# Kernel optimization log

Measured on AMD Instinct MI355X. Metric: run time of the kernel, lower is better.

Reference implementation:

```python
import jax, jax.numpy as jnp
import numpy as np

N_NODES = 50000
N_EDGES = 400000
IN_DIM = 512
OUT_DIM = 512


def setup_inputs() -> dict:
    key = jax.random.key(0)
    k1, k2, k3, k4 = jax.random.split(key, 4)
    x = jax.random.normal(k1, (N_NODES, IN_DIM), dtype=jnp.float32)
    edge_index = jax.random.randint(k2, (2, N_EDGES), 0, N_NODES, dtype=jnp.int64)
    # nn.Linear(in_dim, out_dim): weight [out, in], bias [out]
    W = jax.random.normal(k3, (OUT_DIM, IN_DIM), dtype=jnp.float32) / np.sqrt(IN_DIM)
    b = jax.random.normal(k4, (OUT_DIM,), dtype=jnp.float32) * 0.01
    return {"x": x, "edge_index": edge_index, "W": W, "b": b}


def reference(x, edge_index, W, b):
    n = x.shape[0]
    loops = jnp.arange(n, dtype=edge_index.dtype)
    row = jnp.concatenate([edge_index[0], loops])  # src
    col = jnp.concatenate([edge_index[1], loops])  # dst
    # degree from row counts (matches torch.bincount(row)); self-loops ensure deg >= 1
    deg = jax.ops.segment_sum(jnp.ones(row.shape[0], dtype=x.dtype), row, num_segments=n)
    dis = jax.lax.rsqrt(deg)  # deg^-0.5
    norm = dis[row] * dis[col]  # [E+N]
    h = x @ W.T + b  # [N, out_dim]
    # out[dst] += norm * h[src], fused gather-scale-scatter
    out = jax.ops.segment_sum(norm[:, None] * h[row], col, num_segments=n)
    return jax.nn.relu(out)
```

## Files before the change

kernel.cpp:

```cpp
#include <hip/hip_runtime.h>
#include <hip/hip_bf16.h>

#define K_DIM 512
#define N_DIM 512

typedef __attribute__((ext_vector_type(8))) short s8v;
typedef __attribute__((ext_vector_type(4))) short s4v;
typedef __attribute__((ext_vector_type(4))) float f4v;

__device__ __forceinline__ short f2bf(float f) {
  union { float f; unsigned u; } v; v.f = f;
  unsigned r = (v.u + 0x7FFFu + ((v.u >> 16) & 1u)) >> 16;
  return (short)r;
}
__device__ __forceinline__ float bflo(unsigned u) {
  union { unsigned u; float f; } v; v.u = u << 16; return v.f;
}
__device__ __forceinline__ float bfhi(unsigned u) {
  union { unsigned u; float f; } v; v.u = u & 0xffff0000u; return v.f;
}

__device__ __forceinline__ void gload16(const void* g, void* l) {
  __builtin_amdgcn_global_load_lds(
      (const __attribute__((address_space(1))) void*)g,
      (__attribute__((address_space(3))) void*)l, 16, 0, 0);
}

__global__ void k_flag(const int* __restrict__ e32, int* __restrict__ flag) {
  int t = threadIdx.x;
  int v = e32[2 * t + 1];
  unsigned long long m = __ballot(v == 0);
  if (t == 0) flag[0] = (m == ~0ULL) ? 1 : 0;
}

__global__ void k_convW(const float* __restrict__ W, short* __restrict__ Wb) {
  int i = (blockIdx.x * blockDim.x + threadIdx.x) * 4;
  float4 f = *(const float4*)(W + i);
  s4v s; s[0] = f2bf(f.x); s[1] = f2bf(f.y); s[2] = f2bf(f.z); s[3] = f2bf(f.w);
  *(s4v*)(Wb + i) = s;
}

__global__ void k_hist(const int* __restrict__ e32, const int* __restrict__ flag,
                       int* __restrict__ outdeg, int* __restrict__ indeg, int E) {
  int i = blockIdx.x * blockDim.x + threadIdx.x;
  if (i >= E) return;
  int st = flag[0] ? 2 : 1;
  int r = e32[(size_t)i * st];
  int c = e32[(size_t)(E + i) * st];
  atomicAdd(&outdeg[r], 1);
  atomicAdd(&indeg[c], 1);
}

__global__ void k_dis(const int* __restrict__ outdeg, float* __restrict__ dis, int n) {
  int i = blockIdx.x * blockDim.x + threadIdx.x;
  if (i < n) dis[i] = rsqrtf((float)(outdeg[i] + 1));
}

__global__ void k_scan_a(const int* __restrict__ in, int* __restrict__ part, int n) {
  __shared__ int sm[256];
  int i = blockIdx.x * 256 + threadIdx.x;
  sm[threadIdx.x] = (i < n) ? in[i] : 0;
  __syncthreads();
  for (int off = 128; off > 0; off >>= 1) {
    if (threadIdx.x < off) sm[threadIdx.x] += sm[threadIdx.x + off];
    __syncthreads();
  }
  if (threadIdx.x == 0) part[blockIdx.x] = sm[0];
}

__global__ void k_scan_b(int* __restrict__ part, int nb, int* __restrict__ row_start, int n) {
  __shared__ int sm[256];
  int t = threadIdx.x;
  int v = (t < nb) ? part[t] : 0;
  sm[t] = v; __syncthreads();
  for (int off = 1; off < 256; off <<= 1) {
    int a = (t >= off) ? sm[t - off] : 0;
    __syncthreads();
    sm[t] += a;
    __syncthreads();
  }
  part[t] = sm[t] - v;
  if (t == 255) row_start[n] = sm[255];
}

__global__ void k_scan_c(const int* __restrict__ in, const int* __restrict__ part,
                         int* __restrict__ row_start, int* __restrict__ cursor, int n) {
  __shared__ int sm[256];
  int i = blockIdx.x * 256 + threadIdx.x;
  int v = (i < n) ? in[i] : 0;
  sm[threadIdx.x] = v; __syncthreads();
  for (int off = 1; off < 256; off <<= 1) {
    int a = (threadIdx.x >= off) ? sm[threadIdx.x - off] : 0;
    __syncthreads();
    sm[threadIdx.x] += a;
    __syncthreads();
  }
  if (i < n) {
    int excl = part[blockIdx.x] + sm[threadIdx.x] - v;
    row_start[i] = excl;
    cursor[i] = excl;
  }
}

__global__ void k_fill(const int* __restrict__ e32, const int* __restrict__ flag,
                       int* __restrict__ cursor, int* __restrict__ csr, int E) {
  int i = blockIdx.x * blockDim.x + threadIdx.x;
  if (i >= E) return;
  int st = flag[0] ? 2 : 1;
  int r = e32[(size_t)i * st];
  int c = e32[(size_t)(E + i) * st];
  int p = atomicAdd(&cursor[c], 1);
  csr[p] = r;
}

__global__ __launch_bounds__(256) void k_gemm(const float* __restrict__ x,
    const short* __restrict__ Wb, const float* __restrict__ bias,
    short* __restrict__ h, int M) {
  __shared__ __align__(16) short As[2][128][40];
  __shared__ __align__(16) short Bs[2][128][32];
  const int n0 = blockIdx.x * 128;
  const int m0 = blockIdx.y * 128;
  const int tid = threadIdx.x;
  const int lane = tid & 63;
  const int wv = tid >> 6, wr = wv >> 1, wc = wv & 1;
  const int la = lane & 15, lg = lane >> 4;
  const int sr = tid >> 1, sc = (tid & 1) * 16;
  const float* xrow = x + (size_t)(m0 + sr) * K_DIM + sc;
  const bool aok = (m0 + sr) < M;
  const short* bsrc = Wb + (size_t)(n0 + (tid >> 2)) * K_DIM + (tid & 3) * 8;
  char* bdst0 = (char*)&Bs[0][0][0] + wv * 1024;
  char* bdst1 = (char*)&Bs[1][0][0] + wv * 1024;

  f4v acc[4][4] = {};

  gload16(bsrc, bdst0);
  gload16(bsrc + (size_t)64 * K_DIM, bdst0 + 4096);
  {
    float4 f0{}, f1{}, f2{}, f3{};
    if (aok) {
      f0 = *(const float4*)(xrow);
      f1 = *(const float4*)(xrow + 4);
      f2 = *(const float4*)(xrow + 8);
      f3 = *(const float4*)(xrow + 12);
    }
    s8v v0, v1;
    v0[0] = f2bf(f0.x); v0[1] = f2bf(f0.y); v0[2] = f2bf(f0.z); v0[3] = f2bf(f0.w);
    v0[4] = f2bf(f1.x); v0[5] = f2bf(f1.y); v0[6] = f2bf(f1.z); v0[7] = f2bf(f1.w);
    v1[0] = f2bf(f2.x); v1[1] = f2bf(f2.y); v1[2] = f2bf(f2.z); v1[3] = f2bf(f2.w);
    v1[4] = f2bf(f3.x); v1[5] = f2bf(f3.y); v1[6] = f2bf(f3.z); v1[7] = f2bf(f3.w);
    *(s8v*)&As[0][sr][sc] = v0;
    *(s8v*)&As[0][sr][sc + 8] = v1;
  }
  __syncthreads();

  for (int kt = 0; kt < 16; ++kt) {
    const int cur = kt & 1;
    const int nxt = cur ^ 1;
    float4 f0{}, f1{}, f2{}, f3{};
    if (kt < 15) {
      const int kk = (kt + 1) * 32;
      char* bd = cur ? bdst0 : bdst1;
      gload16(bsrc + kk, bd);
      gload16(bsrc + kk + (size_t)64 * K_DIM, bd + 4096);
      if (aok) {
        f0 = *(const float4*)(xrow + kk);
        f1 = *(const float4*)(xrow + kk + 4);
        f2 = *(const float4*)(xrow + kk + 8);
        f3 = *(const float4*)(xrow + kk + 12);
      }
    }
    s8v a0 = *(const s8v*)&As[cur][64 * wr + la][8 * lg];
    s8v a1 = *(const s8v*)&As[cur][64 * wr + 16 + la][8 * lg];
    s8v a2 = *(const s8v*)&As[cur][64 * wr + 32 + la][8 * lg];
    s8v a3 = *(const s8v*)&As[cur][64 * wr + 48 + la][8 * lg];
    s8v b0 = *(const s8v*)&Bs[cur][64 * wc + la][8 * lg];
    s8v b1 = *(const s8v*)&Bs[cur][64 * wc + 16 + la][8 * lg];
    s8v b2 = *(const s8v*)&Bs[cur][64 * wc + 32 + la][8 * lg];
    s8v b3 = *(const s8v*)&Bs[cur][64 * wc + 48 + la][8 * lg];
    acc[0][0] = __builtin_amdgcn_mfma_f32_16x16x32_bf16(a0, b0, acc[0][0], 0, 0, 0);
    acc[0][1] = __builtin_amdgcn_mfma_f32_16x16x32_bf16(a0, b1, acc[0][1], 0, 0, 0);
    acc[0][2] = __builtin_amdgcn_mfma_f32_16x16x32_bf16(a0, b2, acc[0][2], 0, 0, 0);
    acc[0][3] = __builtin_amdgcn_mfma_f32_16x16x32_bf16(a0, b3, acc[0][3], 0, 0, 0);
    acc[1][0] = __builtin_amdgcn_mfma_f32_16x16x32_bf16(a1, b0, acc[1][0], 0, 0, 0);
    acc[1][1] = __builtin_amdgcn_mfma_f32_16x16x32_bf16(a1, b1, acc[1][1], 0, 0, 0);
    acc[1][2] = __builtin_amdgcn_mfma_f32_16x16x32_bf16(a1, b2, acc[1][2], 0, 0, 0);
    acc[1][3] = __builtin_amdgcn_mfma_f32_16x16x32_bf16(a1, b3, acc[1][3], 0, 0, 0);
    acc[2][0] = __builtin_amdgcn_mfma_f32_16x16x32_bf16(a2, b0, acc[2][0], 0, 0, 0);
    acc[2][1] = __builtin_amdgcn_mfma_f32_16x16x32_bf16(a2, b1, acc[2][1], 0, 0, 0);
    acc[2][2] = __builtin_amdgcn_mfma_f32_16x16x32_bf16(a2, b2, acc[2][2], 0, 0, 0);
    acc[2][3] = __builtin_amdgcn_mfma_f32_16x16x32_bf16(a2, b3, acc[2][3], 0, 0, 0);
    acc[3][0] = __builtin_amdgcn_mfma_f32_16x16x32_bf16(a3, b0, acc[3][0], 0, 0, 0);
    acc[3][1] = __builtin_amdgcn_mfma_f32_16x16x32_bf16(a3, b1, acc[3][1], 0, 0, 0);
    acc[3][2] = __builtin_amdgcn_mfma_f32_16x16x32_bf16(a3, b2, acc[3][2], 0, 0, 0);
    acc[3][3] = __builtin_amdgcn_mfma_f32_16x16x32_bf16(a3, b3, acc[3][3], 0, 0, 0);
    if (kt < 15) {
      s8v v0, v1;
      v0[0] = f2bf(f0.x); v0[1] = f2bf(f0.y); v0[2] = f2bf(f0.z); v0[3] = f2bf(f0.w);
      v0[4] = f2bf(f1.x); v0[5] = f2bf(f1.y); v0[6] = f2bf(f1.z); v0[7] = f2bf(f1.w);
      v1[0] = f2bf(f2.x); v1[1] = f2bf(f2.y); v1[2] = f2bf(f2.z); v1[3] = f2bf(f2.w);
      v1[4] = f2bf(f3.x); v1[5] = f2bf(f3.y); v1[6] = f2bf(f3.z); v1[7] = f2bf(f3.w);
      *(s8v*)&As[nxt][sr][sc] = v0;
      *(s8v*)&As[nxt][sr][sc + 8] = v1;
    }
    __syncthreads();
  }

  #pragma unroll
  for (int i = 0; i < 4; ++i) {
    #pragma unroll
    for (int j = 0; j < 4; ++j) {
      int col = n0 + 64 * wc + 16 * j + la;
      float bv = bias[col];
      #pragma unroll
      for (int r = 0; r < 4; ++r) {
        int row = m0 + 64 * wr + 16 * i + lg * 4 + r;
        if (row < M) h[(size_t)row * N_DIM + col] = f2bf(acc[i][j][r] + bv);
      }
    }
  }
}

__device__ __forceinline__ void acc8(float* acc, uint4 rv, float wv) {
  acc[0] += wv * bflo(rv.x); acc[1] += wv * bfhi(rv.x);
  acc[2] += wv * bflo(rv.y); acc[3] += wv * bfhi(rv.y);
  acc[4] += wv * bflo(rv.z); acc[5] += wv * bfhi(rv.z);
  acc[6] += wv * bflo(rv.w); acc[7] += wv * bfhi(rv.w);
}

__global__ __launch_bounds__(256) void k_scatter(const short* __restrict__ h,
    const float* __restrict__ dis, const int* __restrict__ row_start,
    const int* __restrict__ csr, float* __restrict__ out, int n) {
  int v = blockIdx.x * 4 + (threadIdx.x >> 6);
  if (v >= n) return;
  int lane = threadIdx.x & 63;
  const short* hl = h + lane * 8;
  float dv = dis[v];
  float acc[8];
  {
    uint4 r = *(const uint4*)(hl + (size_t)v * N_DIM);
    float w = dv * dv;
    acc[0] = w * bflo(r.x); acc[1] = w * bfhi(r.x);
    acc[2] = w * bflo(r.y); acc[3] = w * bfhi(r.y);
    acc[4] = w * bflo(r.z); acc[5] = w * bfhi(r.z);
    acc[6] = w * bflo(r.w); acc[7] = w * bfhi(r.w);
  }
  int s = __builtin_amdgcn_readfirstlane(row_start[v]);
  int e = __builtin_amdgcn_readfirstlane(row_start[v + 1]);
  int idx = s;
  for (; idx + 2 <= e; idx += 2) {
    int s0 = csr[idx];
    int s1 = csr[idx + 1];
    float w0 = dis[s0] * dv;
    float w1 = dis[s1] * dv;
    uint4 r0 = *(const uint4*)(hl + (size_t)s0 * N_DIM);
    uint4 r1 = *(const uint4*)(hl + (size_t)s1 * N_DIM);
    acc8(acc, r0, w0);
    acc8(acc, r1, w1);
  }
  if (idx < e) {
    int s0 = csr[idx];
    float w0 = dis[s0] * dv;
    uint4 r0 = *(const uint4*)(hl + (size_t)s0 * N_DIM);
    acc8(acc, r0, w0);
  }
  float* op = out + (size_t)v * N_DIM + lane * 8;
  float4 o0, o1;
  o0.x = fmaxf(acc[0], 0.f); o0.y = fmaxf(acc[1], 0.f);
  o0.z = fmaxf(acc[2], 0.f); o0.w = fmaxf(acc[3], 0.f);
  o1.x = fmaxf(acc[4], 0.f); o1.y = fmaxf(acc[5], 0.f);
  o1.z = fmaxf(acc[6], 0.f); o1.w = fmaxf(acc[7], 0.f);
  *(float4*)op = o0;
  *(float4*)(op + 4) = o1;
}

extern "C" void kernel_launch(void* const* d_in, const int* in_sizes, int n_in,
                              void* d_out, int out_size, void* d_ws, size_t ws_size,
                              hipStream_t stream) {
  const float* x = (const float*)d_in[0];
  const int* e32 = (const int*)d_in[1];
  const float* W = (const float*)d_in[2];
  const float* bias = (const float*)d_in[3];
  float* out = (float*)d_out;
  int M = in_sizes[0] / K_DIM;
  int E = in_sizes[1] / 2;

  char* ws = (char*)d_ws;
  size_t off = 0;
  auto alloc = [&](size_t bytes) {
    void* p = ws + off;
    off = (off + bytes + 255) & ~(size_t)255;
    return p;
  };
  short* Wb      = (short*)alloc((size_t)N_DIM * K_DIM * 2);
  short* h       = (short*)alloc((size_t)M * N_DIM * 2);
  float* dis     = (float*)alloc((size_t)M * 4);
  int*   outdeg  = (int*)alloc((size_t)M * 4);
  int*   indeg   = (int*)alloc((size_t)M * 4);
  int*   rstart  = (int*)alloc((size_t)(M + 1) * 4);
  int*   cursor  = (int*)alloc((size_t)M * 4);
  int*   part    = (int*)alloc(256 * 4);
  int*   csr     = (int*)alloc((size_t)E * 4);
  int*   flag    = (int*)alloc(4);
  if (off > ws_size) return;

  (void)hipMemsetAsync(outdeg, 0, (size_t)M * 4, stream);
  (void)hipMemsetAsync(indeg, 0, (size_t)M * 4, stream);
  k_flag<<<1, 64, 0, stream>>>(e32, flag);
  k_convW<<<(N_DIM * K_DIM / 4 + 255) / 256, 256, 0, stream>>>(W, Wb);
  k_hist<<<(E + 255) / 256, 256, 0, stream>>>(e32, flag, outdeg, indeg, E);
  k_dis<<<(M + 255) / 256, 256, 0, stream>>>(outdeg, dis, M);
  int nscan = (M + 255) / 256;
  k_scan_a<<<nscan, 256, 0, stream>>>(indeg, part, M);
  k_scan_b<<<1, 256, 0, stream>>>(part, nscan, rstart, M);
  k_scan_c<<<nscan, 256, 0, stream>>>(indeg, part, rstart, cursor, M);
  k_fill<<<(E + 255) / 256, 256, 0, stream>>>(e32, flag, cursor, csr, E);
  k_gemm<<<dim3(N_DIM / 128, (M + 127) / 128), 256, 0, stream>>>(x, Wb, bias, h, M);
  k_scatter<<<(M + 3) / 4, 256, 0, stream>>>(h, dis, rstart, csr, out, M);
}
```

Before: 242.9 us.

## Deepen GEMM K-tile to 64 with XOR-swizzled B LDS, XCD grid remap, unroll gather

The GEMM now loads 64-wide K tiles, halving the loop trips and barriers. The B tile in LDS uses an XOR swizzle on 16-byte chunks to avoid bank conflicts, the As row padding grows, and the grid is flattened and remapped so consecutive tiles land on the same XCD for L2 reuse. The scatter kernel's gather loop is unrolled to 4 neighbors to raise memory-level parallelism. LDS use and register pressure go up, which may reduce occupancy.

```diff
diff --git a/kernel.cpp b/kernel.cpp
--- a/kernel.cpp
+++ b/kernel.cpp
@@ -116,91 +116,100 @@
 __global__ __launch_bounds__(256) void k_gemm(const float* __restrict__ x,
     const short* __restrict__ Wb, const float* __restrict__ bias,
     short* __restrict__ h, int M) {
-  __shared__ __align__(16) short As[2][128][40];
-  __shared__ __align__(16) short Bs[2][128][32];
-  const int n0 = blockIdx.x * 128;
-  const int m0 = blockIdx.y * 128;
+  __shared__ __align__(16) short As[2][128][72];
+  __shared__ __align__(16) short Bs[2][128][64];
+  int nwg = gridDim.x;
+  int orig = blockIdx.x;
+  int q8 = nwg >> 3, r8 = nwg & 7;
+  int xcd = orig & 7, pos = orig >> 3;
+  int swz = (xcd < r8 ? xcd * (q8 + 1) : r8 * (q8 + 1) + (xcd - r8) * q8) + pos;
+  const int n0 = (swz & 3) * 128;
+  const int m0 = (swz >> 2) * 128;
+
   const int tid = threadIdx.x;
   const int lane = tid & 63;
   const int wv = tid >> 6, wr = wv >> 1, wc = wv & 1;
   const int la = lane & 15, lg = lane >> 4;
-  const int sr = tid >> 1, sc = (tid & 1) * 16;
+  const int sr = tid >> 1, sc = (tid & 1) * 32;
   const float* xrow = x + (size_t)(m0 + sr) * K_DIM + sc;
   const bool aok = (m0 + sr) < M;
-  const short* bsrc = Wb + (size_t)(n0 + (tid >> 2)) * K_DIM + (tid & 3) * 8;
-  char* bdst0 = (char*)&Bs[0][0][0] + wv * 1024;
-  char* bdst1 = (char*)&Bs[1][0][0] + wv * 1024;
+  size_t goff[4];
+  int doff[4];
+  #pragma unroll
+  for (int qq = 0; qq < 4; ++qq) {
+    int i = qq * 256 + tid;
+    int row = i >> 3, ch = i & 7;
+    int sch = ch ^ (row & 7);
+    goff[qq] = (size_t)(n0 + row) * K_DIM + sch * 8;
+    doff[qq] = (qq * 256 + (tid & 0xC0)) * 16;
+  }
+  const int bxor = la & 7;
 
   f4v acc[4][4] = {};
 
-  gload16(bsrc, bdst0);
-  gload16(bsrc + (size_t)64 * K_DIM, bdst0 + 4096);
+  #pragma unroll
+  for (int qq = 0; qq < 4; ++qq)
+    gload16(Wb + goff[qq], (char*)&Bs[0][0][0] + doff[qq]);
   {
-    float4 f0{}, f1{}, f2{}, f3{};
-    if (aok) {
-      f0 = *(const float4*)(xrow);
-      f1 = *(const float4*)(xrow + 4);
-      f2 = *(const float4*)(xrow + 8);
-      f3 = *(const float4*)(xrow + 12);
-    }
-    s8v v0, v1;
-    v0[0] = f2bf(f0.x); v0[1] = f2bf(f0.y); v0[2] = f2bf(f0.z); v0[3] = f2bf(f0.w);
-    v0[4] = f2bf(f1.x); v0[5] = f2bf(f1.y); v0[6] = f2bf(f1.z); v0[7] = f2bf(f1.w);
-    v1[0] = f2bf(f2.x); v1[1] = f2bf(f2.y); v1[2] = f2bf(f2.z); v1[3] = f2bf(f2.w);
-    v1[4] = f2bf(f3.x); v1[5] = f2bf(f3.y); v1[6] = f2bf(f3.z); v1[7] = f2bf(f3.w);
-    *(s8v*)&As[0][sr][sc] = v0;
-    *(s8v*)&As[0][sr][sc + 8] = v1;
+    float4 f[8];
+    #pragma unroll
+    for (int t = 0; t < 8; ++t)
+      f[t] = aok ? *(const float4*)(xrow + 4 * t) : float4{0, 0, 0, 0};
+    #pragma unroll
+    for (int mq = 0; mq < 4; ++mq) {
+      s8v v;
+      v[0] = f2bf(f[2 * mq].x);     v[1] = f2bf(f[2 * mq].y);
+      v[2] = f2bf(f[2 * mq].z);     v[3] = f2bf(f[2 * mq].w);
+      v[4] = f2bf(f[2 * mq + 1].x); v[5] = f2bf(f[2 * mq + 1].y);
+      v[6] = f2bf(f[2 * mq + 1].z); v[7] = f2bf(f[2 * mq + 1].w);
+      *(s8v*)&As[0][sr][sc + 8 * mq] = v;
+    }
   }
   __syncthreads();
 
-  for (int kt = 0; kt < 16; ++kt) {
+  for (int kt = 0; kt < 8; ++kt) {
     const int cur = kt & 1;
     const int nxt = cur ^ 1;
-    float4 f0{}, f1{}, f2{}, f3{};
-    if (kt < 15) {
-      const int kk = (kt + 1) * 32;
-      char* bd = cur ? bdst0 : bdst1;
-      gload16(bsrc + kk, bd);
-      gload16(bsrc + kk + (size_t)64 * K_DIM, bd + 4096);
-      if (aok) {
-        f0 = *(const float4*)(xrow + kk);
-        f1 = *(const float4*)(xrow + kk + 4);
-        f2 = *(const float4*)(xrow + kk + 8);
-        f3 = *(const float4*)(xrow + kk + 12);
+    float4 f[8];
+    if (kt < 7) {
+      const int kk = (kt + 1) * 64;
+      char* bb = (char*)&Bs[nxt][0][0];
+      #pragma unroll
+      for (int qq = 0; qq < 4; ++qq)
+        gload16(Wb + goff[qq] + kk, bb + doff[qq]);
+      #pragma unroll
+      for (int t = 0; t < 8; ++t)
+        f[t] = aok ? *(const float4*)(xrow + kk + 4 * t) : float4{0, 0, 0, 0};
+    }
+    const char* bbase = (const char*)&Bs[cur][0][0];
+    #pragma unroll
+    for (int s = 0; s < 2; ++s) {
+      s8v af[4], bf[4];
+      #pragma unroll
+      for (int i = 0; i < 4; ++i)
+        af[i] = *(const s8v*)&As[cur][64 * wr + 16 * i + la][s * 32 + 8 * lg];
+      #pragma unroll
+      for (int j = 0; j < 4; ++j) {
+        int row = 64 * wc + 16 * j + la;
+        int off = row * 128 + ((((s << 2) | lg) ^ bxor) << 4);
+        bf[j] = *(const s8v*)(bbase + off);
       }
-    }
-    s8v a0 = *(const s8v*)&As[cur][64 * wr + la][8 * lg];
-    s8v a1 = *(const s8v*)&As[cur][64 * wr + 16 + la][8 * lg];
-    s8v a2 = *(const s8v*)&As[cur][64 * wr + 32 + la][8 * lg];
-    s8v a3 = *(const s8v*)&As[cur][64 * wr + 48 + la][8 * lg];
-    s8v b0 = *(const s8v*)&Bs[cur][64 * wc + la][8 * lg];
-    s8v b1 = *(const s8v*)&Bs[cur][64 * wc + 16 + la][8 * lg];
-    s8v b2 = *(const s8v*)&Bs[cur][64 * wc + 32 + la][8 * lg];
-    s8v b3 = *(const s8v*)&Bs[cur][64 * wc + 48 + la][8 * lg];
-    acc[0][0] = __builtin_amdgcn_mfma_f32_16x16x32_bf16(a0, b0, acc[0][0], 0, 0, 0);
-    acc[0][1] = __builtin_amdgcn_mfma_f32_16x16x32_bf16(a0, b1, acc[0][1], 0, 0, 0);
-    acc[0][2] = __builtin_amdgcn_mfma_f32_16x16x32_bf16(a0, b2, acc[0][2], 0, 0, 0);
-    acc[0][3] = __builtin_amdgcn_mfma_f32_16x16x32_bf16(a0, b3, acc[0][3], 0, 0, 0);
-    acc[1][0] = __builtin_amdgcn_mfma_f32_16x16x32_bf16(a1, b0, acc[1][0], 0, 0, 0);
-    acc[1][1] = __builtin_amdgcn_mfma_f32_16x16x32_bf16(a1, b1, acc[1][1], 0, 0, 0);
-    acc[1][2] = __builtin_amdgcn_mfma_f32_16x16x32_bf16(a1, b2, acc[1][2], 0, 0, 0);
-    acc[1][3] = __builtin_amdgcn_mfma_f32_16x16x32_bf16(a1, b3, acc[1][3], 0, 0, 0);
-    acc[2][0] = __builtin_amdgcn_mfma_f32_16x16x32_bf16(a2, b0, acc[2][0], 0, 0, 0);
-    acc[2][1] = __builtin_amdgcn_mfma_f32_16x16x32_bf16(a2, b1, acc[2][1], 0, 0, 0);
-    acc[2][2] = __builtin_amdgcn_mfma_f32_16x16x32_bf16(a2, b2, acc[2][2], 0, 0, 0);
-    acc[2][3] = __builtin_amdgcn_mfma_f32_16x16x32_bf16(a2, b3, acc[2][3], 0, 0, 0);
-    acc[3][0] = __builtin_amdgcn_mfma_f32_16x16x32_bf16(a3, b0, acc[3][0], 0, 0, 0);
-    acc[3][1] = __builtin_amdgcn_mfma_f32_16x16x32_bf16(a3, b1, acc[3][1], 0, 0, 0);
-    acc[3][2] = __builtin_amdgcn_mfma_f32_16x16x32_bf16(a3, b2, acc[3][2], 0, 0, 0);
-    acc[3][3] = __builtin_amdgcn_mfma_f32_16x16x32_bf16(a3, b3, acc[3][3], 0, 0, 0);
-    if (kt < 15) {
-      s8v v0, v1;
-      v0[0] = f2bf(f0.x); v0[1] = f2bf(f0.y); v0[2] = f2bf(f0.z); v0[3] = f2bf(f0.w);
-      v0[4] = f2bf(f1.x); v0[5] = f2bf(f1.y); v0[6] = f2bf(f1.z); v0[7] = f2bf(f1.w);
-      v1[0] = f2bf(f2.x); v1[1] = f2bf(f2.y); v1[2] = f2bf(f2.z); v1[3] = f2bf(f2.w);
-      v1[4] = f2bf(f3.x); v1[5] = f2bf(f3.y); v1[6] = f2bf(f3.z); v1[7] = f2bf(f3.w);
-      *(s8v*)&As[nxt][sr][sc] = v0;
-      *(s8v*)&As[nxt][sr][sc + 8] = v1;
+      #pragma unroll
+      for (int i = 0; i < 4; ++i)
+        #pragma unroll
+        for (int j = 0; j < 4; ++j)
+          acc[i][j] = __builtin_amdgcn_mfma_f32_16x16x32_bf16(af[i], bf[j], acc[i][j], 0, 0, 0);
+    }
+    if (kt < 7) {
+      #pragma unroll
+      for (int mq = 0; mq < 4; ++mq) {
+        s8v v;
+        v[0] = f2bf(f[2 * mq].x);     v[1] = f2bf(f[2 * mq].y);
+        v[2] = f2bf(f[2 * mq].z);     v[3] = f2bf(f[2 * mq].w);
+        v[4] = f2bf(f[2 * mq + 1].x); v[5] = f2bf(f[2 * mq + 1].y);
+        v[6] = f2bf(f[2 * mq + 1].z); v[7] = f2bf(f[2 * mq + 1].w);
+        *(s8v*)&As[nxt][sr][sc + 8 * mq] = v;
+      }
     }
     __syncthreads();
   }
@@ -247,17 +256,20 @@
   int s = __builtin_amdgcn_readfirstlane(row_start[v]);
   int e = __builtin_amdgcn_readfirstlane(row_start[v + 1]);
   int idx = s;
-  for (; idx + 2 <= e; idx += 2) {
-    int s0 = csr[idx];
-    int s1 = csr[idx + 1];
-    float w0 = dis[s0] * dv;
-    float w1 = dis[s1] * dv;
+  for (; idx + 4 <= e; idx += 4) {
+    int s0 = csr[idx], s1 = csr[idx + 1], s2 = csr[idx + 2], s3 = csr[idx + 3];
+    float w0 = dis[s0] * dv, w1 = dis[s1] * dv;
+    float w2 = dis[s2] * dv, w3 = dis[s3] * dv;
     uint4 r0 = *(const uint4*)(hl + (size_t)s0 * N_DIM);
     uint4 r1 = *(const uint4*)(hl + (size_t)s1 * N_DIM);
+    uint4 r2 = *(const uint4*)(hl + (size_t)s2 * N_DIM);
+    uint4 r3 = *(const uint4*)(hl + (size_t)s3 * N_DIM);
     acc8(acc, r0, w0);
     acc8(acc, r1, w1);
-  }
-  if (idx < e) {
+    acc8(acc, r2, w2);
+    acc8(acc, r3, w3);
+  }
+  for (; idx < e; ++idx) {
     int s0 = csr[idx];
     float w0 = dis[s0] * dv;
     uint4 r0 = *(const uint4*)(hl + (size_t)s0 * N_DIM);
@@ -314,6 +326,7 @@
   k_scan_b<<<1, 256, 0, stream>>>(part, nscan, rstart, M);
   k_scan_c<<<nscan, 256, 0, stream>>>(indeg, part, rstart, cursor, M);
   k_fill<<<(E + 255) / 256, 256, 0, stream>>>(e32, flag, cursor, csr, E);
-  k_gemm<<<dim3(N_DIM / 128, (M + 127) / 128), 256, 0, stream>>>(x, Wb, bias, h, M);
+  int nmc = (M + 127) / 128;
+  k_gemm<<<nmc * 4, 256, 0, stream>>>(x, Wb, bias, h, M);
   k_scatter<<<(M + 3) / 4, 256, 0, stream>>>(h, dis, rstart, csr, out, M);
 }
```

Result: slower. 262.7 us (+8.2%).
